# Kernel optimization log

Measured on AMD Instinct MI355X. Metric: run time of the kernel, lower is better.

The kernel has to match this reference:

```python
import jax, jax.numpy as jnp
import numpy as np

B, N, C = 16, 256, 2048
CLASSES = (16, 5, 5)
H = len(CLASSES)
EPS = 1e-5


def setup_inputs() -> dict:
    key = jax.random.key(0)
    ks = iter(jax.random.split(key, 32))
    d = {}
    d["features"] = jax.random.normal(next(ks), (B, N, C), dtype=jnp.float32)
    # 3 hidden conv layers per head; 3x3 conv on 1x1 spatial == linear with center tap.
    # Stack the H heads' weights: [H, C_out, C_in].
    std = 1.0 / np.sqrt(C)
    for i in (1, 2, 3):
        d[f"W{i}"] = jax.random.normal(next(ks), (H, C, C), dtype=jnp.float32) * std
        d[f"g{i}"] = 1.0 + 0.1 * jax.random.normal(next(ks), (H, C), dtype=jnp.float32)
        d[f"b{i}"] = 0.1 * jax.random.normal(next(ks), (H, C), dtype=jnp.float32)
        d[f"m{i}"] = 0.1 * jax.random.normal(next(ks), (H, C), dtype=jnp.float32)
        d[f"v{i}"] = jax.random.uniform(next(ks), (H, C), dtype=jnp.float32, minval=0.5, maxval=1.5)
    # Final 1x1 conv per head: [c_i, C] weight + [c_i] bias (output dims differ per head).
    for h, c in enumerate(CLASSES):
        d[f"Wf{h}"] = jax.random.normal(next(ks), (c, C), dtype=jnp.float32) * std
        d[f"bf{h}"] = 0.1 * jax.random.normal(next(ks), (c,), dtype=jnp.float32)
    return d


def _bn_relu(y, g, b, m, v):
    # y: [H, M, C]; per-head inference-mode BN folded to scale/shift, then ReLU.
    scale = g / jnp.sqrt(v + EPS)          # [H, C]
    shift = b - m * scale                  # [H, C]
    return jax.nn.relu(y * scale[:, None, :] + shift[:, None, :])


def reference(features, W1, g1, b1, m1, v1, W2, g2, b2, m2, v2, W3, g3, b3, m3, v3,
              Wf0, bf0, Wf1, bf1, Wf2, bf2):
    Bs, Ns, Cs = features.shape
    x = features.reshape(Bs * Ns, Cs)                       # [M, C]
    y = jnp.einsum("mc,hdc->hmd", x, W1)                    # [H, M, C]
    y = _bn_relu(y, g1, b1, m1, v1)
    y = jnp.einsum("hmc,hdc->hmd", y, W2)
    y = _bn_relu(y, g2, b2, m2, v2)
    y = jnp.einsum("hmc,hdc->hmd", y, W3)
    y = _bn_relu(y, g3, b3, m3, v3)
    outs = [y[h] @ Wf.T + bf for h, (Wf, bf) in enumerate([(Wf0, bf0), (Wf1, bf1), (Wf2, bf2)])]
    cl = jnp.concatenate(outs, axis=-1)                     # [M, sum(classes)]
    return cl.reshape(Bs, Ns, cl.shape[-1])
```

## Files before the change

kernel.cpp:

```cpp
#include <hip/hip_runtime.h>
#include <hip/hip_bf16.h>

typedef __attribute__((ext_vector_type(8))) short short8;
typedef __attribute__((ext_vector_type(4))) float f32x4;

#define BN_EPS 1e-5f
#define MROWS 4096
#define CDIM 2048
#define NKT 32

#define SB() __builtin_amdgcn_sched_barrier(0)

__device__ __forceinline__ void gload_lds16(const void* g, void* l) {
  __builtin_amdgcn_global_load_lds(
      (const __attribute__((address_space(1))) void*)g,
      (__attribute__((address_space(3))) void*)l, 16, 0, 0);
}

__device__ __forceinline__ unsigned short bf16u(float x) {
  __hip_bfloat16 h = __float2bfloat16(x);
  return *(unsigned short*)&h;
}

__global__ __launch_bounds__(256) void cvt_f32_bf16(const float* __restrict__ in,
                                                    unsigned short* __restrict__ out,
                                                    int n4) {
  int idx = blockIdx.x * blockDim.x + threadIdx.x;
  int stride = gridDim.x * blockDim.x;
  for (int i = idx; i < n4; i += stride) {
    float4 vv = ((const float4*)in)[i];
    ushort4 o;
    o.x = bf16u(vv.x); o.y = bf16u(vv.y); o.z = bf16u(vv.z); o.w = bf16u(vv.w);
    ((ushort4*)out)[i] = o;
  }
}

__global__ __launch_bounds__(256) void cvt2_f32_bf16(
    const float* __restrict__ inA, unsigned short* __restrict__ outA, int nA4,
    const float* __restrict__ inB, unsigned short* __restrict__ outB, int nB4) {
  int idx = blockIdx.x * blockDim.x + threadIdx.x;
  int stride = gridDim.x * blockDim.x;
  int tot = nA4 + nB4;
  for (int i = idx; i < tot; i += stride) {
    const float4* src; ushort4* dst; int k;
    if (i < nA4) { src = (const float4*)inA; dst = (ushort4*)outA; k = i; }
    else         { src = (const float4*)inB; dst = (ushort4*)outB; k = i - nA4; }
    float4 vv = src[k];
    ushort4 o;
    o.x = bf16u(vv.x); o.y = bf16u(vv.y); o.z = bf16u(vv.z); o.w = bf16u(vv.w);
    dst[k] = o;
  }
}

__global__ __launch_bounds__(512, 2) void gemm128_ring(
    const __hip_bfloat16* __restrict__ A, long long a_hstride,
    const __hip_bfloat16* __restrict__ W,
    const float* __restrict__ gp, const float* __restrict__ bp,
    const float* __restrict__ mp, const float* __restrict__ vp,
    __hip_bfloat16* __restrict__ out)
{
  __shared__ __hip_bfloat16 sm[73728];

  const int tid  = threadIdx.x;
  const int w    = tid >> 6;
  const int lane = tid & 63;

  const int bid = blockIdx.x;
  const int swz = (bid & 7) * 96 + (bid >> 3);
  const int h   = swz >> 8;
  const int rem = swz & 255;
  const int mt  = rem >> 3;
  const int nt  = rem & 7;

  const __hip_bfloat16* Abase = A + (size_t)h * (size_t)a_hstride + (size_t)(mt * 128) * CDIM;
  const __hip_bfloat16* Bbase = W + ((size_t)h * CDIM + (size_t)(nt * 256)) * CDIM;

  const int row0 = tid >> 3;
  const int ch0  = (tid & 7) ^ (row0 & 7);
  const __hip_bfloat16* aSrc = Abase + (size_t)row0 * CDIM + ch0 * 8;
  const __hip_bfloat16* bSrc = Bbase + (size_t)row0 * CDIM + ch0 * 8;

  const int wm = w >> 2, wn = w & 3;
  const int fr = lane & 15, fg = lane >> 4;
  const int offs0 = fr * 64 + ((fg ^ (fr & 7)) << 3);
  const int offs1 = fr * 64 + (((fg + 4) ^ (fr & 7)) << 3);
  const int aoffs0 = wm * 4096 + offs0;
  const int aoffs1 = wm * 4096 + offs1;
  const int boffs0 = 8192 + wn * 4096 + offs0;
  const int boffs1 = 8192 + wn * 4096 + offs1;

  auto SA_ = [&](int buf, int t) {
    __hip_bfloat16* dp = &sm[buf + tid * 8];
    gload_lds16(aSrc + t * 64, dp);
    gload_lds16(aSrc + (size_t)64 * CDIM + t * 64, dp + 4096);
  };
  auto SB0 = [&](int buf, int t) {
    __hip_bfloat16* dp = &sm[buf + 8192 + tid * 8];
    gload_lds16(bSrc + t * 64, dp);
    gload_lds16(bSrc + (size_t)64 * CDIM + t * 64, dp + 4096);
  };
  auto SB1 = [&](int buf, int t) {
    __hip_bfloat16* dp = &sm[buf + 8192 + 8192 + tid * 8];
    gload_lds16(bSrc + (size_t)128 * CDIM + t * 64, dp);
    gload_lds16(bSrc + (size_t)192 * CDIM + t * 64, dp + 4096);
  };

  f32x4 acc[4][4] = {};
  short8 Af[4], Ap[4], B0[2], B1[2], B0p[2], B1p[2];

#define LDA4(dst, base)                                                  \
  _Pragma("unroll") for (int i_ = 0; i_ < 4; ++i_)                       \
    dst[i_] = *(const short8*)&sm[(base) + i_ * 1024];
#define LDB2(dst, base, j0)                                              \
  _Pragma("unroll") for (int j_ = 0; j_ < 2; ++j_)                       \
    dst[j_] = *(const short8*)&sm[(base) + ((j0) + j_) * 1024];

#define MFMA_G(joff, Aset, Bset)                                         \
  __builtin_amdgcn_s_setprio(1);                                         \
  _Pragma("unroll") for (int i_ = 0; i_ < 4; ++i_)                       \
  _Pragma("unroll") for (int j_ = 0; j_ < 2; ++j_)                       \
    acc[i_][j_ + joff] = __builtin_amdgcn_mfma_f32_16x16x32_bf16(        \
        Aset[i_], Bset[j_], acc[i_][j_ + joff], 0, 0, 0);                \
  __builtin_amdgcn_s_setprio(0);

  SA_(0, 0); SB0(0, 0); SB1(0, 0);
  SA_(24576, 1); SB0(24576, 1); SB1(24576, 1);
  asm volatile("s_waitcnt vmcnt(6)" ::: "memory");
  SB();
  __builtin_amdgcn_s_barrier();
  SB();
  LDA4(Af, 0 + aoffs0);
  LDB2(B0, 0 + boffs0, 0);
  LDB2(B1, 0 + boffs0, 2);
  SB();

  int oc = 0, on = 24576, os = 49152;
  for (int t = 0; t < NKT; ++t) {
    MFMA_G(0, Af, B0); SB();
    LDB2(B0p, oc + boffs1, 0); SB();
    MFMA_G(2, Af, B1); SB();
    LDA4(Ap, oc + aoffs1);
    if (t + 2 < NKT) SA_(os, t + 2);
    SB();
    MFMA_G(0, Ap, B0p); SB();
    LDB2(B1p, oc + boffs1, 2);
    if (t + 2 < NKT) SB0(os, t + 2);
    SB();
    if (t + 1 < NKT) {
      if (t + 2 < NKT) { asm volatile("s_waitcnt vmcnt(4) lgkmcnt(0)" ::: "memory"); }
      else             { asm volatile("s_waitcnt vmcnt(0) lgkmcnt(0)" ::: "memory"); }
      SB();
      __builtin_amdgcn_s_barrier();
      SB();
    }
    MFMA_G(2, Ap, B1p); SB();
    if (t + 2 < NKT) SB1(os, t + 2);
    if (t + 1 < NKT) {
      LDA4(Af, on + aoffs0);
      LDB2(B0, on + boffs0, 0);
      LDB2(B1, on + boffs0, 2);
    }
    SB();
    const int tmp = oc; oc = on; on = os; os = tmp;
  }

  const float* gh = gp + h * CDIM;
  const float* bh = bp + h * CDIM;
  const float* mh = mp + h * CDIM;
  const float* vh = vp + h * CDIM;
  const int colBase = nt * 256 + wn * 64 + fr;
  const int rowBase = mt * 128 + wm * 64 + fg * 4;
#pragma unroll
  for (int j = 0; j < 4; ++j) {
    const int col = colBase + j * 16;
    const float sc = gh[col] / sqrtf(vh[col] + BN_EPS);
    const float sh = bh[col] - mh[col] * sc;
#pragma unroll
    for (int i = 0; i < 4; ++i) {
      const int row = rowBase + i * 16;
#pragma unroll
      for (int rr = 0; rr < 4; ++rr) {
        float val = acc[i][j][rr] * sc + sh;
        val = val > 0.f ? val : 0.f;
        out[((size_t)h * MROWS + row + rr) * CDIM + col] = __float2bfloat16(val);
      }
    }
  }
}

__global__ __launch_bounds__(256) void pack_wf(
    const float* __restrict__ Wf0, const float* __restrict__ Wf1,
    const float* __restrict__ Wf2, __hip_bfloat16* __restrict__ Wfb) {
  int idx = blockIdx.x * 256 + threadIdx.x;
  if (idx >= 3 * 16 * CDIM) return;
  int h = idx / (16 * CDIM);
  int rem = idx - h * 16 * CDIM;
  int j = rem / CDIM;
  int k = rem - j * CDIM;
  float v = 0.f;
  if (h == 0)            v = Wf0[j * CDIM + k];
  else if (h == 1)       { if (j < 5) v = Wf1[j * CDIM + k]; }
  else                   { if (j < 5) v = Wf2[j * CDIM + k]; }
  Wfb[idx] = __float2bfloat16(v);
}

__global__ __launch_bounds__(512) void final_mfma(
    const __hip_bfloat16* __restrict__ act,
    const __hip_bfloat16* __restrict__ Wfb,
    const float* __restrict__ bf0, const float* __restrict__ bf1,
    const float* __restrict__ bf2, float* __restrict__ out)
{
  __shared__ float red[8][3][256];
  const int tid  = threadIdx.x;
  const int w    = tid >> 6;
  const int lane = tid & 63;
  const int r0   = blockIdx.x * 16;
  const int fr   = lane & 15;
  const int fk   = (lane >> 4) * 8;
  const int kbase = w * 256 + fk;

  f32x4 acc[3] = {};
  const __hip_bfloat16* aRow = act + (size_t)(r0 + fr) * CDIM + kbase;
  const __hip_bfloat16* bRow = Wfb + (size_t)fr * CDIM + kbase;
#pragma unroll
  for (int ks = 0; ks < 8; ++ks) {
    const int k = ks * 32;
#pragma unroll
    for (int h = 0; h < 3; ++h) {
      short8 a = *(const short8*)(aRow + (size_t)h * MROWS * CDIM + k);
      short8 b = *(const short8*)(bRow + h * 16 * CDIM + k);
      acc[h] = __builtin_amdgcn_mfma_f32_16x16x32_bf16(a, b, acc[h], 0, 0, 0);
    }
  }

  const int rb = (lane >> 4) * 4;
#pragma unroll
  for (int h = 0; h < 3; ++h)
#pragma unroll
    for (int r = 0; r < 4; ++r)
      red[w][h][(rb + r) * 16 + fr] = acc[h][r];
  __syncthreads();

  for (int e = tid; e < 768; e += 512) {
    const int h = e >> 8, idx = e & 255;
    const int row = idx >> 4, col = idx & 15;
    float s = 0.f;
#pragma unroll
    for (int w2 = 0; w2 < 8; ++w2) s += red[w2][h][idx];
    float* orow = out + (size_t)(r0 + row) * 26;
    if (h == 0)                 orow[col]      = s + bf0[col];
    else if (h == 1) { if (col < 5) orow[16 + col] = s + bf1[col]; }
    else             { if (col < 5) orow[21 + col] = s + bf2[col]; }
  }
}

extern "C" void kernel_launch(void* const* d_in, const int* in_sizes, int n_in,
                              void* d_out, int out_size, void* d_ws, size_t ws_size,
                              hipStream_t stream) {
  const float* feat = (const float*)d_in[0];
  const float* W1 = (const float*)d_in[1];
  const float* g1 = (const float*)d_in[2];
  const float* b1 = (const float*)d_in[3];
  const float* m1 = (const float*)d_in[4];
  const float* v1 = (const float*)d_in[5];
  const float* W2 = (const float*)d_in[6];
  const float* g2 = (const float*)d_in[7];
  const float* b2 = (const float*)d_in[8];
  const float* m2 = (const float*)d_in[9];
  const float* v2 = (const float*)d_in[10];
  const float* W3 = (const float*)d_in[11];
  const float* g3 = (const float*)d_in[12];
  const float* b3 = (const float*)d_in[13];
  const float* m3 = (const float*)d_in[14];
  const float* v3 = (const float*)d_in[15];
  const float* Wf0 = (const float*)d_in[16];
  const float* bf0 = (const float*)d_in[17];
  const float* Wf1 = (const float*)d_in[18];
  const float* bf1 = (const float*)d_in[19];
  const float* Wf2 = (const float*)d_in[20];
  const float* bf2 = (const float*)d_in[21];
  float* out = (float*)d_out;

  char* ws = (char*)d_ws;
  __hip_bfloat16* wbuf = (__hip_bfloat16*)ws;
  __hip_bfloat16* actA = (__hip_bfloat16*)(ws + 25165824);
  __hip_bfloat16* actB = (__hip_bfloat16*)(ws + 25165824 + 50331648);
  __hip_bfloat16* xb   = actB;
  __hip_bfloat16* Wfb  = wbuf;

  const int nW4 = (3 * CDIM * CDIM) / 4;
  const int nX4 = (MROWS * CDIM) / 4;
  const long long hstride = (long long)MROWS * CDIM;

  cvt2_f32_bf16<<<2048, 256, 0, stream>>>(feat, (unsigned short*)xb, nX4,
                                          W1, (unsigned short*)wbuf, nW4);
  gemm128_ring<<<768, 512, 0, stream>>>(xb, 0LL, wbuf, g1, b1, m1, v1, actA);

  cvt_f32_bf16<<<2048, 256, 0, stream>>>(W2, (unsigned short*)wbuf, nW4);
  gemm128_ring<<<768, 512, 0, stream>>>(actA, hstride, wbuf, g2, b2, m2, v2, actB);

  cvt_f32_bf16<<<2048, 256, 0, stream>>>(W3, (unsigned short*)wbuf, nW4);
  gemm128_ring<<<768, 512, 0, stream>>>(actB, hstride, wbuf, g3, b3, m3, v3, actA);

  pack_wf<<<384, 256, 0, stream>>>(Wf0, Wf1, Wf2, Wfb);
  final_mfma<<<256, 512, 0, stream>>>(actA, Wfb, bf0, bf1, bf2, out);
}
```

Measured before the change: 355.1 us.

## Fuse next-layer weight conversion into GEMM epilogue and convert final weights inline

Each GEMM block now loads its slice of the next layer's fp32 weights after the main loop and writes bf16 copies into a second weight buffer, so the standalone conversion launches between layers go away. The weight buffers are double-buffered so the current layer's weights aren't overwritten. The final projection reads fp32 Wf directly and converts to bf16 in registers, masking heads with 5 classes, which removes the pack kernel. The cost is extra register pressure (8 float4 held across the epilogue) and a larger workspace requirement, with a fallback path if the workspace is too small.

```diff
diff --git a/kernel.cpp b/kernel.cpp
--- a/kernel.cpp
+++ b/kernel.cpp
@@ -20,6 +20,14 @@
 __device__ __forceinline__ unsigned short bf16u(float x) {
   __hip_bfloat16 h = __float2bfloat16(x);
   return *(unsigned short*)&h;
+}
+__device__ __forceinline__ short8 cvt8(float4 a, float4 b) {
+  short8 r;
+  r[0] = (short)bf16u(a.x); r[1] = (short)bf16u(a.y);
+  r[2] = (short)bf16u(a.z); r[3] = (short)bf16u(a.w);
+  r[4] = (short)bf16u(b.x); r[5] = (short)bf16u(b.y);
+  r[6] = (short)bf16u(b.z); r[7] = (short)bf16u(b.w);
+  return r;
 }
 
 __global__ __launch_bounds__(256) void cvt_f32_bf16(const float* __restrict__ in,
@@ -57,7 +65,8 @@
     const __hip_bfloat16* __restrict__ W,
     const float* __restrict__ gp, const float* __restrict__ bp,
     const float* __restrict__ mp, const float* __restrict__ vp,
-    __hip_bfloat16* __restrict__ out)
+    __hip_bfloat16* __restrict__ out,
+    const float* __restrict__ cvtSrc, unsigned short* __restrict__ cvtDst)
 {
   __shared__ __hip_bfloat16 sm[73728];
 
@@ -164,6 +173,14 @@
     const int tmp = oc; oc = on; on = os; os = tmp;
   }
 
+  float4 cw[8];
+  if (cvtSrc) {
+    const float4* csrc = (const float4*)cvtSrc + (size_t)bid * 4096 + tid;
+#pragma unroll
+    for (int q = 0; q < 8; ++q) cw[q] = csrc[q * 512];
+  }
+  SB();
+
   const float* gh = gp + h * CDIM;
   const float* bh = bp + h * CDIM;
   const float* mh = mp + h * CDIM;
@@ -186,29 +203,25 @@
       }
     }
   }
-}
-
-__global__ __launch_bounds__(256) void pack_wf(
-    const float* __restrict__ Wf0, const float* __restrict__ Wf1,
-    const float* __restrict__ Wf2, __hip_bfloat16* __restrict__ Wfb) {
-  int idx = blockIdx.x * 256 + threadIdx.x;
-  if (idx >= 3 * 16 * CDIM) return;
-  int h = idx / (16 * CDIM);
-  int rem = idx - h * 16 * CDIM;
-  int j = rem / CDIM;
-  int k = rem - j * CDIM;
-  float v = 0.f;
-  if (h == 0)            v = Wf0[j * CDIM + k];
-  else if (h == 1)       { if (j < 5) v = Wf1[j * CDIM + k]; }
-  else                   { if (j < 5) v = Wf2[j * CDIM + k]; }
-  Wfb[idx] = __float2bfloat16(v);
-}
-
-__global__ __launch_bounds__(512) void final_mfma(
+
+  if (cvtSrc) {
+    ushort4* cdst = (ushort4*)cvtDst + (size_t)bid * 4096 + tid;
+#pragma unroll
+    for (int q = 0; q < 8; ++q) {
+      float4 v = cw[q];
+      ushort4 o;
+      o.x = bf16u(v.x); o.y = bf16u(v.y); o.z = bf16u(v.z); o.w = bf16u(v.w);
+      cdst[q * 512] = o;
+    }
+  }
+}
+
+__global__ __launch_bounds__(512) void final_mfma_raw(
     const __hip_bfloat16* __restrict__ act,
-    const __hip_bfloat16* __restrict__ Wfb,
-    const float* __restrict__ bf0, const float* __restrict__ bf1,
-    const float* __restrict__ bf2, float* __restrict__ out)
+    const float* __restrict__ Wf0, const float* __restrict__ bf0,
+    const float* __restrict__ Wf1, const float* __restrict__ bf1,
+    const float* __restrict__ Wf2, const float* __restrict__ bf2,
+    float* __restrict__ out)
 {
   __shared__ float red[8][3][256];
   const int tid  = threadIdx.x;
@@ -221,15 +234,29 @@
 
   f32x4 acc[3] = {};
   const __hip_bfloat16* aRow = act + (size_t)(r0 + fr) * CDIM + kbase;
-  const __hip_bfloat16* bRow = Wfb + (size_t)fr * CDIM + kbase;
+  const float* w0p = Wf0 + (size_t)fr * CDIM + kbase;
+  const float* w1p = Wf1 + (size_t)fr * CDIM + kbase;
+  const float* w2p = Wf2 + (size_t)fr * CDIM + kbase;
+  const short8 zro = {0, 0, 0, 0, 0, 0, 0, 0};
 #pragma unroll
   for (int ks = 0; ks < 8; ++ks) {
     const int k = ks * 32;
-#pragma unroll
-    for (int h = 0; h < 3; ++h) {
-      short8 a = *(const short8*)(aRow + (size_t)h * MROWS * CDIM + k);
-      short8 b = *(const short8*)(bRow + h * 16 * CDIM + k);
-      acc[h] = __builtin_amdgcn_mfma_f32_16x16x32_bf16(a, b, acc[h], 0, 0, 0);
+    {
+      short8 a = *(const short8*)(aRow + k);
+      short8 b = cvt8(*(const float4*)(w0p + k), *(const float4*)(w0p + k + 4));
+      acc[0] = __builtin_amdgcn_mfma_f32_16x16x32_bf16(a, b, acc[0], 0, 0, 0);
+    }
+    {
+      short8 a = *(const short8*)(aRow + (size_t)MROWS * CDIM + k);
+      short8 b = zro;
+      if (fr < 5) b = cvt8(*(const float4*)(w1p + k), *(const float4*)(w1p + k + 4));
+      acc[1] = __builtin_amdgcn_mfma_f32_16x16x32_bf16(a, b, acc[1], 0, 0, 0);
+    }
+    {
+      short8 a = *(const short8*)(aRow + (size_t)2 * MROWS * CDIM + k);
+      short8 b = zro;
+      if (fr < 5) b = cvt8(*(const float4*)(w2p + k), *(const float4*)(w2p + k + 4));
+      acc[2] = __builtin_amdgcn_mfma_f32_16x16x32_bf16(a, b, acc[2], 0, 0, 0);
     }
   }
 
@@ -281,27 +308,47 @@
   const float* bf2 = (const float*)d_in[21];
   float* out = (float*)d_out;
 
-  char* ws = (char*)d_ws;
-  __hip_bfloat16* wbuf = (__hip_bfloat16*)ws;
-  __hip_bfloat16* actA = (__hip_bfloat16*)(ws + 25165824);
-  __hip_bfloat16* actB = (__hip_bfloat16*)(ws + 25165824 + 50331648);
-  __hip_bfloat16* xb   = actB;
-  __hip_bfloat16* Wfb  = wbuf;
-
+  const size_t WB = 25165824;
+  const size_t AB = 50331648;
   const int nW4 = (3 * CDIM * CDIM) / 4;
   const int nX4 = (MROWS * CDIM) / 4;
   const long long hstride = (long long)MROWS * CDIM;
-
-  cvt2_f32_bf16<<<2048, 256, 0, stream>>>(feat, (unsigned short*)xb, nX4,
-                                          W1, (unsigned short*)wbuf, nW4);
-  gemm128_ring<<<768, 512, 0, stream>>>(xb, 0LL, wbuf, g1, b1, m1, v1, actA);
-
-  cvt_f32_bf16<<<2048, 256, 0, stream>>>(W2, (unsigned short*)wbuf, nW4);
-  gemm128_ring<<<768, 512, 0, stream>>>(actA, hstride, wbuf, g2, b2, m2, v2, actB);
-
-  cvt_f32_bf16<<<2048, 256, 0, stream>>>(W3, (unsigned short*)wbuf, nW4);
-  gemm128_ring<<<768, 512, 0, stream>>>(actB, hstride, wbuf, g3, b3, m3, v3, actA);
-
-  pack_wf<<<384, 256, 0, stream>>>(Wf0, Wf1, Wf2, Wfb);
-  final_mfma<<<256, 512, 0, stream>>>(actA, Wfb, bf0, bf1, bf2, out);
-}
+  char* ws = (char*)d_ws;
+
+  __hip_bfloat16* actA;
+
+  if (ws_size >= 2 * WB + 2 * AB) {
+    __hip_bfloat16* wbufA = (__hip_bfloat16*)ws;
+    __hip_bfloat16* wbufB = (__hip_bfloat16*)(ws + WB);
+    actA                  = (__hip_bfloat16*)(ws + 2 * WB);
+    __hip_bfloat16* actB  = (__hip_bfloat16*)(ws + 2 * WB + AB);
+    __hip_bfloat16* xb    = actB;
+
+    cvt2_f32_bf16<<<2048, 256, 0, stream>>>(feat, (unsigned short*)xb, nX4,
+                                            W1, (unsigned short*)wbufA, nW4);
+    gemm128_ring<<<768, 512, 0, stream>>>(xb, 0LL, wbufA, g1, b1, m1, v1, actA,
+                                          W2, (unsigned short*)wbufB);
+    gemm128_ring<<<768, 512, 0, stream>>>(actA, hstride, wbufB, g2, b2, m2, v2, actB,
+                                          W3, (unsigned short*)wbufA);
+    gemm128_ring<<<768, 512, 0, stream>>>(actB, hstride, wbufA, g3, b3, m3, v3, actA,
+                                          nullptr, nullptr);
+  } else {
+    __hip_bfloat16* wbuf = (__hip_bfloat16*)ws;
+    actA                 = (__hip_bfloat16*)(ws + WB);
+    __hip_bfloat16* actB = (__hip_bfloat16*)(ws + WB + AB);
+    __hip_bfloat16* xb   = actB;
+
+    cvt2_f32_bf16<<<2048, 256, 0, stream>>>(feat, (unsigned short*)xb, nX4,
+                                            W1, (unsigned short*)wbuf, nW4);
+    gemm128_ring<<<768, 512, 0, stream>>>(xb, 0LL, wbuf, g1, b1, m1, v1, actA,
+                                          nullptr, nullptr);
+    cvt_f32_bf16<<<2048, 256, 0, stream>>>(W2, (unsigned short*)wbuf, nW4);
+    gemm128_ring<<<768, 512, 0, stream>>>(actA, hstride, wbuf, g2, b2, m2, v2, actB,
+                                          nullptr, nullptr);
+    cvt_f32_bf16<<<2048, 256, 0, stream>>>(W3, (unsigned short*)wbuf, nW4);
+    gemm128_ring<<<768, 512, 0, stream>>>(actB, hstride, wbuf, g3, b3, m3, v3, actA,
+                                          nullptr, nullptr);
+  }
+
+  final_mfma_raw<<<256, 512, 0, stream>>>(actA, Wf0, bf0, Wf1, bf1, Wf2, bf2, out);
+}
```

New measurement: 353.6 us. About the same (-0.4%).
